# Optimization experiments

Hardware: AMD Instinct MI355X
Metric: run time of the kernel (lower is better)

## Reference

```python
import jax, jax.numpy as jnp
import numpy as np

PROTON = 1.00782503207
WATER = 18.0105646863
HUBER_DELTA = 0.2


def setup_inputs() -> dict:
    key = jax.random.key(0)
    k1, k2, k3, k4 = jax.random.split(key, 4)
    B, L, V, M = 512, 64, 28, 1024
    # probability distribution over vocab per position
    u = jax.random.uniform(k1, (B, L, V), dtype=jnp.float32)
    sequence_probs = u / u.sum(-1, keepdims=True)
    # observed spectrum: m/z values up to ~4000 Da, random intensities
    observed_masses = jax.random.uniform(k2, (B, M), dtype=jnp.float32) * 4000.0
    observed_intensities = jax.random.uniform(k3, (B, M), dtype=jnp.float32)
    peak_mask = jnp.ones((B, M), dtype=bool)
    # amino-acid monoisotopic masses buffer (realistic 57..186 Da range)
    aa_masses = 57.0 + jax.random.uniform(k4, (V,), dtype=jnp.float32) * 129.0
    return {
        "sequence_probs": sequence_probs,
        "observed_masses": observed_masses,
        "observed_intensities": observed_intensities,
        "peak_mask": peak_mask,
        "aa_masses": aa_masses,
    }


def _theoretical_peaks(sequence_probs, aa_masses):
    # expected residue mass per position: E[m_i] = sum_aa P(aa_i) * mass(aa)
    r = jnp.einsum("blv,v->bl", sequence_probs, aa_masses)  # (B, L)
    prefix = jnp.cumsum(r, axis=-1)                          # (B, L)
    total = prefix[:, -1:]                                   # (B, 1)
    # b ions: prefix fragments (lengths 1..L-1) + proton
    b_ions = prefix[:, :-1] + PROTON                         # (B, L-1)
    # y ions: suffix fragments + water + proton
    y_ions = total - prefix[:, :-1] + WATER + PROTON         # (B, L-1)
    return jnp.concatenate([b_ions, y_ions], axis=-1)        # (B, 2*(L-1))


def reference(sequence_probs, observed_masses, observed_intensities, peak_mask, aa_masses):
    theoretical = _theoretical_peaks(sequence_probs, aa_masses)    # (B, T)
    # pairwise |theo - obs| distance, then min over theoretical peaks
    distances = jnp.abs(theoretical[:, :, None] - observed_masses[:, None, :])  # (B, T, M)
    min_distances = distances.min(axis=1)                          # (B, M)
    huber = jnp.where(
        min_distances <= HUBER_DELTA,
        0.5 * min_distances ** 2,
        HUBER_DELTA * (min_distances - 0.5 * HUBER_DELTA),
    )
    intensity_norm = observed_intensities / jnp.clip(
        observed_intensities.sum(axis=-1, keepdims=True), 1e-8
    )
    weighted = (huber * intensity_norm * peak_mask.astype(jnp.float32)).sum(axis=-1)  # (B,)
    return weighted.mean()
```

## Files before the change

kernel.cpp:

```cpp
#include <hip/hip_runtime.h>

#define PROTON_F 1.00782503207f
#define WATER_F 18.0105646863f
#define HUBER_DELTA_F 0.2f

constexpr int B = 512;
constexpr int L = 64;
constexpr int V = 28;
constexpr int M = 1024;
constexpr int THREADS = 256;
constexpr int PROW = 29;


__global__ __launch_bounds__(THREADS)
void spectrum_loss_main(const float* __restrict__ probs,
                        const float* __restrict__ obs_mass,
                        const float* __restrict__ obs_int,
                        const int* __restrict__ mask,
                        const float* __restrict__ aa,
                        float* __restrict__ per_b)
{
    const int b = blockIdx.x;
    const int tid = threadIdx.x;
    const int lane = tid & 63;
    const int wave = tid >> 6;

    __shared__ float s_probs[L * PROW];
    __shared__ float s_bA[64];
    __shared__ float s_yA[64];
    __shared__ float s_red[8];

    const size_t obase = (size_t)b * M;
    const float4 om4 = ((const float4*)(obs_mass + obase))[tid];
    const float4 oi4 = ((const float4*)(obs_int + obase))[tid];
    const int4   mk4 = ((const int4*)(mask + obase))[tid];

    const float4* p4 = (const float4*)(probs + (size_t)b * (L * V));
    #pragma unroll
    for (int j = tid; j < (L * V) / 4; j += THREADS) {
        const float4 v = p4[j];
        float* dst = &s_probs[(j / 7) * PROW + (j % 7) * 4];
        dst[0] = v.x; dst[1] = v.y; dst[2] = v.z; dst[3] = v.w;
    }
    __syncthreads();

    if (wave == 0) {
        float r = 0.f;
        #pragma unroll
        for (int c = 0; c < 7; ++c) {
            const float4 a = ((const float4*)aa)[c];
            const float* pr = &s_probs[lane * PROW + c * 4];
            r += pr[0] * a.x + pr[1] * a.y + pr[2] * a.z + pr[3] * a.w;
        }
        float pref = r;
        #pragma unroll
        for (int off = 1; off < 64; off <<= 1) {
            const float t = __shfl_up(pref, off, 64);
            if (lane >= off) pref += t;
        }
        const float total = __shfl(pref, 63, 64);
        s_bA[lane] = (lane < 63) ? pref + PROTON_F : 1e30f;
        if (lane < 63) s_yA[62 - lane] = total - pref + WATER_F + PROTON_F;
        else           s_yA[63] = 1e30f;
    }
    __syncthreads();

    const float omv0 = om4.x, omv1 = om4.y, omv2 = om4.z, omv3 = om4.w;
    int ib0 = 0, ib1 = 0, ib2 = 0, ib3 = 0;
    int iy0 = 0, iy1 = 0, iy2 = 0, iy3 = 0;
    #pragma unroll
    for (int k = 32; k >= 1; k >>= 1) {
        ib0 += (s_bA[ib0 + k - 1] < omv0) ? k : 0;
        ib1 += (s_bA[ib1 + k - 1] < omv1) ? k : 0;
        ib2 += (s_bA[ib2 + k - 1] < omv2) ? k : 0;
        ib3 += (s_bA[ib3 + k - 1] < omv3) ? k : 0;
        iy0 += (s_yA[iy0 + k - 1] < omv0) ? k : 0;
        iy1 += (s_yA[iy1 + k - 1] < omv1) ? k : 0;
        iy2 += (s_yA[iy2 + k - 1] < omv2) ? k : 0;
        iy3 += (s_yA[iy3 + k - 1] < omv3) ? k : 0;
    }
    float mind0, mind1, mind2, mind3;
    {
        float db, dy;
        db = fminf(fabsf(s_bA[ib0] - omv0), fabsf(s_bA[ib0 - (ib0 > 0)] - omv0));
        dy = fminf(fabsf(s_yA[iy0] - omv0), fabsf(s_yA[iy0 - (iy0 > 0)] - omv0));
        mind0 = fminf(db, dy);
        db = fminf(fabsf(s_bA[ib1] - omv1), fabsf(s_bA[ib1 - (ib1 > 0)] - omv1));
        dy = fminf(fabsf(s_yA[iy1] - omv1), fabsf(s_yA[iy1 - (iy1 > 0)] - omv1));
        mind1 = fminf(db, dy);
        db = fminf(fabsf(s_bA[ib2] - omv2), fabsf(s_bA[ib2 - (ib2 > 0)] - omv2));
        dy = fminf(fabsf(s_yA[iy2] - omv2), fabsf(s_yA[iy2 - (iy2 > 0)] - omv2));
        mind2 = fminf(db, dy);
        db = fminf(fabsf(s_bA[ib3] - omv3), fabsf(s_bA[ib3 - (ib3 > 0)] - omv3));
        dy = fminf(fabsf(s_yA[iy3] - omv3), fabsf(s_yA[iy3 - (iy3 > 0)] - omv3));
        mind3 = fminf(db, dy);
    }

    float wsum = 0.f, isum = 0.f;
    {
        float d, h;
        d = mind0; h = (d <= HUBER_DELTA_F) ? 0.5f * d * d
                                            : HUBER_DELTA_F * (d - 0.5f * HUBER_DELTA_F);
        wsum += h * oi4.x * (float)mk4.x;  isum += oi4.x;
        d = mind1; h = (d <= HUBER_DELTA_F) ? 0.5f * d * d
                                            : HUBER_DELTA_F * (d - 0.5f * HUBER_DELTA_F);
        wsum += h * oi4.y * (float)mk4.y;  isum += oi4.y;
        d = mind2; h = (d <= HUBER_DELTA_F) ? 0.5f * d * d
                                            : HUBER_DELTA_F * (d - 0.5f * HUBER_DELTA_F);
        wsum += h * oi4.z * (float)mk4.z;  isum += oi4.z;
        d = mind3; h = (d <= HUBER_DELTA_F) ? 0.5f * d * d
                                            : HUBER_DELTA_F * (d - 0.5f * HUBER_DELTA_F);
        wsum += h * oi4.w * (float)mk4.w;  isum += oi4.w;
    }

    #pragma unroll
    for (int off = 32; off > 0; off >>= 1) {
        wsum += __shfl_down(wsum, off, 64);
        isum += __shfl_down(isum, off, 64);
    }
    if (lane == 0) { s_red[wave] = wsum; s_red[4 + wave] = isum; }
    __syncthreads();

    if (tid == 0) {
        const float w = s_red[0] + s_red[1] + s_red[2] + s_red[3];
        const float i = s_red[4] + s_red[5] + s_red[6] + s_red[7];
        per_b[b] = w / fmaxf(i, 1e-8f);
    }
}

__global__ __launch_bounds__(64)
void final_reduce_wave(const float* __restrict__ per_b, float* __restrict__ out)
{
    const int lane = threadIdx.x;
    const float4 a = ((const float4*)per_b)[lane * 2];
    const float4 c = ((const float4*)per_b)[lane * 2 + 1];
    float v = (a.x + a.y) + (a.z + a.w) + (c.x + c.y) + (c.z + c.w);
    #pragma unroll
    for (int off = 32; off > 0; off >>= 1)
        v += __shfl_down(v, off, 64);
    if (lane == 0) out[0] = v * (1.0f / (float)B);
}

extern "C" void kernel_launch(void* const* d_in, const int* in_sizes, int n_in,
                              void* d_out, int out_size, void* d_ws, size_t ws_size,
                              hipStream_t stream)
{
    const float* probs = (const float*)d_in[0];
    const float* omass = (const float*)d_in[1];
    const float* oint  = (const float*)d_in[2];
    const int*   pmask = (const int*)d_in[3];
    const float* aa    = (const float*)d_in[4];
    float* out  = (float*)d_out;
    float* perb = (float*)d_ws;

    spectrum_loss_main<<<B, THREADS, 0, stream>>>(probs, omass, oint, pmask, aa, perb);
    final_reduce_wave<<<1, 64, 0, stream>>>(perb, out);
}
```

Before: 11.20 us.

## Double block threads and read probabilities directly from global in wave 0

The block grows from 256 to 512 threads, so each thread now handles two observed peaks through float2 loads instead of four through float4 loads, which shortens the per-thread search and Huber work. The shared-memory staging of the probability tile and its barrier are removed. Wave 0 instead reads each position's 28 probabilities straight from global memory to form expected residue masses. In exchange, wave 0's global loads are strided per lane rather than coalesced, and there are twice as many waves per block to reduce.

```diff
diff --git a/kernel.cpp b/kernel.cpp
--- a/kernel.cpp
+++ b/kernel.cpp
@@ -8,8 +8,7 @@
 constexpr int L = 64;
 constexpr int V = 28;
 constexpr int M = 1024;
-constexpr int THREADS = 256;
-constexpr int PROW = 29;
+constexpr int THREADS = 512;
 
 
 __global__ __launch_bounds__(THREADS)
@@ -25,32 +24,23 @@
     const int lane = tid & 63;
     const int wave = tid >> 6;
 
-    __shared__ float s_probs[L * PROW];
     __shared__ float s_bA[64];
     __shared__ float s_yA[64];
-    __shared__ float s_red[8];
+    __shared__ float s_red[16];
 
     const size_t obase = (size_t)b * M;
-    const float4 om4 = ((const float4*)(obs_mass + obase))[tid];
-    const float4 oi4 = ((const float4*)(obs_int + obase))[tid];
-    const int4   mk4 = ((const int4*)(mask + obase))[tid];
-
-    const float4* p4 = (const float4*)(probs + (size_t)b * (L * V));
-    #pragma unroll
-    for (int j = tid; j < (L * V) / 4; j += THREADS) {
-        const float4 v = p4[j];
-        float* dst = &s_probs[(j / 7) * PROW + (j % 7) * 4];
-        dst[0] = v.x; dst[1] = v.y; dst[2] = v.z; dst[3] = v.w;
-    }
-    __syncthreads();
+    const float2 om2 = ((const float2*)(obs_mass + obase))[tid];
+    const float2 oi2 = ((const float2*)(obs_int + obase))[tid];
+    const int2   mk2 = ((const int2*)(mask + obase))[tid];
 
     if (wave == 0) {
+        const float* prow = probs + (size_t)b * (L * V) + lane * V;
         float r = 0.f;
         #pragma unroll
         for (int c = 0; c < 7; ++c) {
+            const float4 p = ((const float4*)prow)[c];
             const float4 a = ((const float4*)aa)[c];
-            const float* pr = &s_probs[lane * PROW + c * 4];
-            r += pr[0] * a.x + pr[1] * a.y + pr[2] * a.z + pr[3] * a.w;
+            r += p.x * a.x + p.y * a.y + p.z * a.z + p.w * a.w;
         }
         float pref = r;
         #pragma unroll
@@ -65,21 +55,16 @@
     }
     __syncthreads();
 
-    const float omv0 = om4.x, omv1 = om4.y, omv2 = om4.z, omv3 = om4.w;
-    int ib0 = 0, ib1 = 0, ib2 = 0, ib3 = 0;
-    int iy0 = 0, iy1 = 0, iy2 = 0, iy3 = 0;
+    const float omv0 = om2.x, omv1 = om2.y;
+    int ib0 = 0, ib1 = 0, iy0 = 0, iy1 = 0;
     #pragma unroll
     for (int k = 32; k >= 1; k >>= 1) {
         ib0 += (s_bA[ib0 + k - 1] < omv0) ? k : 0;
         ib1 += (s_bA[ib1 + k - 1] < omv1) ? k : 0;
-        ib2 += (s_bA[ib2 + k - 1] < omv2) ? k : 0;
-        ib3 += (s_bA[ib3 + k - 1] < omv3) ? k : 0;
         iy0 += (s_yA[iy0 + k - 1] < omv0) ? k : 0;
         iy1 += (s_yA[iy1 + k - 1] < omv1) ? k : 0;
-        iy2 += (s_yA[iy2 + k - 1] < omv2) ? k : 0;
-        iy3 += (s_yA[iy3 + k - 1] < omv3) ? k : 0;
     }
-    float mind0, mind1, mind2, mind3;
+    float mind0, mind1;
     {
         float db, dy;
         db = fminf(fabsf(s_bA[ib0] - omv0), fabsf(s_bA[ib0 - (ib0 > 0)] - omv0));
@@ -88,12 +73,6 @@
         db = fminf(fabsf(s_bA[ib1] - omv1), fabsf(s_bA[ib1 - (ib1 > 0)] - omv1));
         dy = fminf(fabsf(s_yA[iy1] - omv1), fabsf(s_yA[iy1 - (iy1 > 0)] - omv1));
         mind1 = fminf(db, dy);
-        db = fminf(fabsf(s_bA[ib2] - omv2), fabsf(s_bA[ib2 - (ib2 > 0)] - omv2));
-        dy = fminf(fabsf(s_yA[iy2] - omv2), fabsf(s_yA[iy2 - (iy2 > 0)] - omv2));
-        mind2 = fminf(db, dy);
-        db = fminf(fabsf(s_bA[ib3] - omv3), fabsf(s_bA[ib3 - (ib3 > 0)] - omv3));
-        dy = fminf(fabsf(s_yA[iy3] - omv3), fabsf(s_yA[iy3 - (iy3 > 0)] - omv3));
-        mind3 = fminf(db, dy);
     }
 
     float wsum = 0.f, isum = 0.f;
@@ -101,16 +80,10 @@
         float d, h;
         d = mind0; h = (d <= HUBER_DELTA_F) ? 0.5f * d * d
                                             : HUBER_DELTA_F * (d - 0.5f * HUBER_DELTA_F);
-        wsum += h * oi4.x * (float)mk4.x;  isum += oi4.x;
+        wsum += h * oi2.x * (float)mk2.x;  isum += oi2.x;
         d = mind1; h = (d <= HUBER_DELTA_F) ? 0.5f * d * d
                                             : HUBER_DELTA_F * (d - 0.5f * HUBER_DELTA_F);
-        wsum += h * oi4.y * (float)mk4.y;  isum += oi4.y;
-        d = mind2; h = (d <= HUBER_DELTA_F) ? 0.5f * d * d
-                                            : HUBER_DELTA_F * (d - 0.5f * HUBER_DELTA_F);
-        wsum += h * oi4.z * (float)mk4.z;  isum += oi4.z;
-        d = mind3; h = (d <= HUBER_DELTA_F) ? 0.5f * d * d
-                                            : HUBER_DELTA_F * (d - 0.5f * HUBER_DELTA_F);
-        wsum += h * oi4.w * (float)mk4.w;  isum += oi4.w;
+        wsum += h * oi2.y * (float)mk2.y;  isum += oi2.y;
     }
 
     #pragma unroll
@@ -118,12 +91,14 @@
         wsum += __shfl_down(wsum, off, 64);
         isum += __shfl_down(isum, off, 64);
     }
-    if (lane == 0) { s_red[wave] = wsum; s_red[4 + wave] = isum; }
+    if (lane == 0) { s_red[wave] = wsum; s_red[8 + wave] = isum; }
     __syncthreads();
 
     if (tid == 0) {
-        const float w = s_red[0] + s_red[1] + s_red[2] + s_red[3];
-        const float i = s_red[4] + s_red[5] + s_red[6] + s_red[7];
+        const float w = (s_red[0] + s_red[1]) + (s_red[2] + s_red[3])
+                      + (s_red[4] + s_red[5]) + (s_red[6] + s_red[7]);
+        const float i = (s_red[8] + s_red[9]) + (s_red[10] + s_red[11])
+                      + (s_red[12] + s_red[13]) + (s_red[14] + s_red[15]);
         per_b[b] = w / fmaxf(i, 1e-8f);
     }
 }
```

Result: no change. 11.29 us (median of 3 runs) (+0.8%).
